# Optimization experiments

Measured on AMD Instinct MI355X. Metric: run time of the kernel, lower is better.

## Reference

```python
import jax, jax.numpy as jnp
import numpy as np

VAR0, VAR1 = 0.1, 0.2          # SSD variances
IOU_THRESH = 0.5
NUM_CLASSES = 21
NEGPOS_RATIO = 3
ALPHA = 1.0


def mid_to_corner(b):
    # [cx,cy,w,h] -> [xmin,ymin,xmax,ymax]
    return jnp.concatenate([b[:, :2] - b[:, 2:] / 2, b[:, :2] + b[:, 2:] / 2], axis=1)


def jaccard(box_a, box_b):
    # box_a [n,4], box_b [P,4] corner form -> IoU [n,P]
    lt = jnp.maximum(box_a[:, None, :2], box_b[None, :, :2])
    rb = jnp.minimum(box_a[:, None, 2:], box_b[None, :, 2:])
    wh = jnp.clip(rb - lt, 0.0)
    inter = wh[..., 0] * wh[..., 1]
    area_a = (box_a[:, 2] - box_a[:, 0]) * (box_a[:, 3] - box_a[:, 1])
    area_b = (box_b[:, 2] - box_b[:, 0]) * (box_b[:, 3] - box_b[:, 1])
    union = area_a[:, None] + area_b[None, :] - inter
    return inter / union


def encode_offset(matched, priors):
    # matched corner form [P,4], priors center form [P,4]
    g_cxcy = ((matched[:, :2] + matched[:, 2:]) / 2 - priors[:, :2]) / (VAR0 * priors[:, 2:])
    g_wh = jnp.log((matched[:, 2:] - matched[:, :2]) / priors[:, 2:]) / VAR1
    return jnp.concatenate([g_cxcy, g_wh], axis=1)


def match_one(gt_box, gt_cls, valid, priors_corner, priors_mid):
    # gt_box [n,4], gt_cls [n], valid [n] bool; priors [P,4]
    n = gt_box.shape[0]
    P = priors_corner.shape[0]
    ovl = jaccard(gt_box, priors_corner)                    # [n,P]
    ovl = jnp.where(valid[:, None], ovl, -1.0)              # mask padded GTs
    best_truth_idx = jnp.argmax(ovl, axis=0)                # [P]
    best_truth_ovl = jnp.max(ovl, axis=0)                   # [P]
    best_prior_idx = jnp.argmax(ovl, axis=1)                # [n]
    bpi = jnp.where(valid, best_prior_idx, P)               # OOB for padded -> dropped
    best_truth_ovl = best_truth_ovl.at[bpi].set(2.0, mode='drop')
    best_truth_idx = best_truth_idx.at[bpi].set(jnp.arange(n), mode='drop')
    matches = gt_box[best_truth_idx]                        # [P,4]
    loc = encode_offset(matches, priors_mid)                # [P,4]
    conf = gt_cls[best_truth_idx].astype(jnp.int32) + 1     # [P]
    conf = jnp.where(best_truth_ovl < IOU_THRESH, 0, conf)
    return loc, conf


def setup_inputs() -> dict:
    key = jax.random.key(0)
    k = jax.random.split(key, 8)
    B, P, C, NMAX = 64, 8732, 21, 50
    confidence = jax.random.normal(k[0], (B, P, C), dtype=jnp.float32)
    location = 0.1 * jax.random.normal(k[1], (B, P, 4), dtype=jnp.float32)
    cxcy = jax.random.uniform(k[2], (P, 2), minval=0.05, maxval=0.95)
    pwh = jax.random.uniform(k[3], (P, 2), minval=0.05, maxval=0.4)
    prior_boxes = jnp.concatenate([cxcy, pwh], axis=1).astype(jnp.float32)
    xymin = jax.random.uniform(k[4], (B, NMAX, 2), minval=0.0, maxval=0.6)
    gwh = jax.random.uniform(k[5], (B, NMAX, 2), minval=0.05, maxval=0.35)
    cls = jax.random.randint(k[6], (B, NMAX), 0, C - 1).astype(jnp.float32)
    labels = jnp.concatenate([xymin, xymin + gwh, cls[..., None]], axis=-1).astype(jnp.float32)
    obj_count = jax.random.randint(k[7], (B, 1), 1, NMAX + 1).astype(jnp.int32)
    return {"confidence": confidence, "location": location,
            "prior_boxes": prior_boxes, "labels": labels, "obj_count": obj_count}


def reference(confidence, location, prior_boxes, labels, obj_count):
    B, P, C = confidence.shape
    NMAX = labels.shape[1]
    priors_corner = mid_to_corner(prior_boxes)
    valid = jnp.arange(NMAX)[None, :] < obj_count            # [B,NMAX]
    loc_t, conf_t = jax.vmap(match_one, in_axes=(0, 0, 0, None, None))(
        labels[..., :4], labels[..., 4], valid, priors_corner, prior_boxes)
    # loc_t [B,P,4] float, conf_t [B,P] int32

    pos = conf_t > 0                                          # [B,P]
    # smooth-L1 over positive anchors (sum reduction)
    d = jnp.abs(location - loc_t)
    sl1 = jnp.where(d < 1.0, 0.5 * d * d, d - 0.5)
    loss_loc = jnp.sum(sl1 * pos[..., None].astype(sl1.dtype))

    # hard negative mining score: global-max logsumexp minus target logit
    bc = confidence.reshape(-1, C)
    x_max = jnp.max(bc)
    lse = jnp.log(jnp.sum(jnp.exp(bc - x_max), axis=1)) + x_max
    tgt_logit = jnp.take_along_axis(bc, conf_t.reshape(-1, 1), axis=1)[:, 0]
    loss_c = (lse - tgt_logit).reshape(B, P)
    loss_c = jnp.where(pos, 0.0, loss_c)
    loss_idx = jnp.argsort(-loss_c, axis=1)                   # descending sort
    idx_rank = jnp.argsort(loss_idx, axis=1)
    num_pos = jnp.sum(pos.astype(jnp.int32), axis=1, keepdims=True)   # [B,1]
    num_neg = jnp.clip(NEGPOS_RATIO * num_pos, None, P - 1)
    neg = idx_rank < num_neg                                  # [B,P]

    # standard cross entropy over selected (pos|neg) anchors, sum reduction
    logp = jax.nn.log_softmax(confidence, axis=-1)            # [B,P,C]
    nll = -jnp.take_along_axis(logp, conf_t[..., None], axis=-1)[..., 0]
    sel = jnp.logical_or(pos, neg)
    loss_conf = jnp.sum(nll * sel.astype(nll.dtype))

    N = jnp.sum(num_pos).astype(confidence.dtype)
    return (ALPHA * loss_loc / N, loss_conf / N)
```

## Files before the change

### kernel.cpp

```cpp
#include <hip/hip_runtime.h>
#include <math.h>

#define Bn 64
#define Pn 8732
#define Cn 21
#define NMAXn 50
#define PX 35

template <int C>
__device__ __forceinline__ float dppf(float x) {
    return __int_as_float(__builtin_amdgcn_update_dpp(0, __float_as_int(x), C, 0xf, 0xf, true));
}
template <int C>
__device__ __forceinline__ int dppi(int x) {
    return __builtin_amdgcn_update_dpp(0, x, C, 0xf, 0xf, true);
}
__device__ __forceinline__ float wave_max_f(float x) {
    x = fmaxf(x, dppf<0x111>(x)); x = fmaxf(x, dppf<0x112>(x));
    x = fmaxf(x, dppf<0x114>(x)); x = fmaxf(x, dppf<0x118>(x));
    x = fmaxf(x, dppf<0x142>(x)); x = fmaxf(x, dppf<0x143>(x));
    return x;
}
__device__ __forceinline__ float wave_sum_f(float x) {
    x += dppf<0x111>(x); x += dppf<0x112>(x); x += dppf<0x114>(x);
    x += dppf<0x118>(x); x += dppf<0x142>(x); x += dppf<0x143>(x);
    return x;
}
__device__ __forceinline__ int wave_sum_i(int x) {
    x += dppi<0x111>(x); x += dppi<0x112>(x); x += dppi<0x114>(x);
    x += dppi<0x118>(x); x += dppi<0x142>(x); x += dppi<0x143>(x);
    return x;
}

__global__ __launch_bounds__(256) void k_bpp(const float* __restrict__ labels,
                                             const int* __restrict__ objc,
                                             const float* __restrict__ priors,
                                             int* __restrict__ match,
                                             unsigned long long* __restrict__ bpk) {
    const int b = blockIdx.y;
    const int px = blockIdx.x;
    const int tid = threadIdx.x;
    const int lane = tid & 63, wid = tid >> 6;
    const int cnt = objc[b];
    const float* lb = labels + b * NMAXn * 5;

    const int p = px * 256 + tid;
    const bool valid = p < Pn;
    const int pcl = valid ? p : (Pn - 1);
    const float4 pr = reinterpret_cast<const float4*>(priors)[pcl];
    const float px0 = pr.x - 0.5f * pr.z, py0 = pr.y - 0.5f * pr.w;
    const float px1 = pr.x + 0.5f * pr.z, py1 = pr.y + 0.5f * pr.w;
    const float parea = (px1 - px0) * (py1 - py0);

    float best = -1.0f;
    int bidx = 0;
    for (int n = 0; n < cnt; ++n) {
        const float gx0 = lb[n * 5 + 0], gy0 = lb[n * 5 + 1];
        const float gx1 = lb[n * 5 + 2], gy1 = lb[n * 5 + 3];
        const float lx = fmaxf(gx0, px0), ly = fmaxf(gy0, py0);
        const float rx = fminf(gx1, px1), ry = fminf(gy1, py1);
        const float w = fmaxf(rx - lx, 0.0f), h = fmaxf(ry - ly, 0.0f);
        const float inter = w * h;
        const float ga = (gx1 - gx0) * (gy1 - gy0);
        const float q = inter / (ga + parea - inter);
        if (q > best) { best = q; bidx = n; }
        const float qr = valid ? q : 0.0f;
        const float m = wave_max_f(qr);
        const float s_q = __int_as_float(__builtin_amdgcn_readlane(__float_as_int(m), 63));
        const unsigned long long mask = __ballot(qr == s_q);
        if (lane == 0) {
            const int first = __ffsll(mask) - 1;
            const int pw = px * 256 + (wid << 6) + first;
            const unsigned long long key =
                ((unsigned long long)__float_as_uint(s_q) << 32) |
                (unsigned long long)(65535 - pw);
            bpk[(size_t)(b * NMAXn + n) * (PX * 4) + px * 4 + wid] = key;
        }
    }
    if (valid) match[(size_t)b * Pn + p] = (bidx << 1) | (best >= 0.5f ? 1 : 0);
}

__global__ __launch_bounds__(64) void k_bpr(const int* __restrict__ objc,
                                            const unsigned long long* __restrict__ bpk,
                                            int* __restrict__ match,
                                            int* __restrict__ done) {
    __shared__ int sbp[NMAXn];
    const int b = blockIdx.x;
    const int tid = threadIdx.x;
    if (b == 0 && tid == 0) *done = 0;
    const int cnt = objc[b];
    if (tid < cnt) {
        const size_t g0 = (size_t)(b * NMAXn + tid) * (PX * 4);
        unsigned long long best = 0ull;
        for (int t = 0; t < PX * 4; ++t) {
            const unsigned long long k = bpk[g0 + t];
            best = (k > best) ? k : best;
        }
        sbp[tid] = 65535 - (int)(best & 0xFFFFull);
    }
    __syncthreads();
    if (tid < cnt) {
        const int myp = sbp[tid];
        bool win = true;
        for (int n2 = tid + 1; n2 < cnt; ++n2) win = win && (sbp[n2] != myp);
        if (win) match[(size_t)b * Pn + myp] = (tid << 1) | 1;
    }
}

__global__ __launch_bounds__(256) void k_main(const float* __restrict__ conf,
                                              const float* __restrict__ loc,
                                              const float* __restrict__ priors,
                                              const float* __restrict__ labels,
                                              const int* __restrict__ match,
                                              float* __restrict__ lc,
                                              float* __restrict__ part_loc,
                                              float* __restrict__ part_nll,
                                              int* __restrict__ part_np) {
    const int b = blockIdx.y;
    const int px = blockIdx.x;
    const int p0 = px * 256;
    const int tid = threadIdx.x;
    const int rows = min(256, Pn - p0);
    const int p = p0 + ((tid < rows) ? tid : 0);
    const size_t gi = (size_t)b * Pn + p;
    const int w = match[gi];

    __shared__ float sconf[256 * Cn];
    __shared__ float lab[NMAXn * 5];
    const float4* src = reinterpret_cast<const float4*>(conf + ((size_t)b * Pn + p0) * Cn);
    const int n4 = rows * Cn / 4;
    for (int i = tid; i < n4; i += 256) reinterpret_cast<float4*>(sconf)[i] = src[i];
    for (int i = tid; i < NMAXn * 5; i += 256) lab[i] = labels[b * NMAXn * 5 + i];
    __syncthreads();

    float my_loc = 0.0f, my_nll = 0.0f;
    int my_np = 0;
    if (tid < rows) {
        const int ti = w >> 1;
        const int ct = (w & 1) ? ((int)lab[ti * 5 + 4] + 1) : 0;
        const float* row = sconf + tid * Cn;
        float m = row[0];
#pragma unroll
        for (int j = 1; j < Cn; ++j) m = fmaxf(m, row[j]);
        float s2 = 0.0f;
#pragma unroll
        for (int j = 0; j < Cn; ++j) s2 += __expf(row[j] - m);
        const float nll = __logf(s2) + m - row[ct];
        if (ct > 0) {
            lc[gi] = 0.0f;
            my_np = 1;
            my_nll = nll;
            const float4 pr = reinterpret_cast<const float4*>(priors)[p];
            const float gx0 = lab[ti * 5 + 0], gy0 = lab[ti * 5 + 1];
            const float gx1 = lab[ti * 5 + 2], gy1 = lab[ti * 5 + 3];
            const float tx = ((gx0 + gx1) * 0.5f - pr.x) / (0.1f * pr.z);
            const float ty = ((gy0 + gy1) * 0.5f - pr.y) / (0.1f * pr.w);
            const float tw = __logf((gx1 - gx0) / pr.z) * 5.0f;
            const float th = __logf((gy1 - gy0) / pr.w) * 5.0f;
            const float4 l = reinterpret_cast<const float4*>(loc)[gi];
            float d;
            d = fabsf(l.x - tx); my_loc += (d < 1.0f) ? 0.5f * d * d : d - 0.5f;
            d = fabsf(l.y - ty); my_loc += (d < 1.0f) ? 0.5f * d * d : d - 0.5f;
            d = fabsf(l.z - tw); my_loc += (d < 1.0f) ? 0.5f * d * d : d - 0.5f;
            d = fabsf(l.w - th); my_loc += (d < 1.0f) ? 0.5f * d * d : d - 0.5f;
        } else {
            lc[gi] = nll;
        }
    }
    my_loc = wave_sum_f(my_loc);
    my_nll = wave_sum_f(my_nll);
    my_np = wave_sum_i(my_np);
    __shared__ float rl[4], rn[4];
    __shared__ int rp[4];
    const int wid = tid >> 6, lane = tid & 63;
    if (lane == 63) { rl[wid] = my_loc; rn[wid] = my_nll; rp[wid] = my_np; }
    __syncthreads();
    if (tid == 0) {
        const int g = b * PX + px;
        part_loc[g] = rl[0] + rl[1] + rl[2] + rl[3];
        part_nll[g] = rn[0] + rn[1] + rn[2] + rn[3];
        part_np[g] = rp[0] + rp[1] + rp[2] + rp[3];
    }
}

__global__ __launch_bounds__(256) void k_neg(const float* __restrict__ lc,
                                             const float* __restrict__ part_loc,
                                             const float* __restrict__ part_nll,
                                             const int* __restrict__ part_np,
                                             float* __restrict__ negsum,
                                             int* __restrict__ done,
                                             float* __restrict__ out) {
    const int b = blockIdx.x;
    const int tid = threadIdx.x;
    const int lane = tid & 63, wid = tid >> 6;
    __shared__ int redc[2][4];
    __shared__ float redf[4], redf2[4];
    __shared__ int redi[4];
    __shared__ int np_sh, islast;

    const int NV = Pn / 4;
    const float4* src = reinterpret_cast<const float4*>(lc + (size_t)b * Pn);
    const float4 sent = make_float4(-1.0f, -1.0f, -1.0f, -1.0f);
    float4 rr[12];
#pragma unroll
    for (int j = 0; j < 12; ++j) {
        const int i = tid + 256 * j;
        rr[j] = (i < NV) ? src[i] : sent;
    }

    if (tid < 64) {
        int npl = (tid < PX) ? part_np[b * PX + tid] : 0;
        npl = wave_sum_i(npl);
        if (tid == 63) np_sh = npl;
    }
    __syncthreads();
    const int k = min(3 * np_sh, Pn - 1);

    unsigned lo = 0u, hi = 0x7F800000u;
#pragma unroll 1
    for (int it = 0; it < 31; ++it) {
        const unsigned mid = lo + ((hi - lo) >> 1);
        const float fm = __uint_as_float(mid);
        int c = 0;
#pragma unroll
        for (int j = 0; j < 12; ++j)
            c += (rr[j].x >= fm) + (rr[j].y >= fm) + (rr[j].z >= fm) + (rr[j].w >= fm);
        c = wave_sum_i(c);
        if (lane == 63) redc[it & 1][wid] = c;
        __syncthreads();
        const int tot = redc[it & 1][0] + redc[it & 1][1]
                      + redc[it & 1][2] + redc[it & 1][3];
        if (tot >= k) lo = mid;
        else hi = mid;
    }
    const float v = __uint_as_float(lo);

    float sm = 0.0f;
    int c = 0;
#pragma unroll
    for (int j = 0; j < 12; ++j) {
        if (rr[j].x > v) { sm += rr[j].x; ++c; }
        if (rr[j].y > v) { sm += rr[j].y; ++c; }
        if (rr[j].z > v) { sm += rr[j].z; ++c; }
        if (rr[j].w > v) { sm += rr[j].w; ++c; }
    }
    sm = wave_sum_f(sm);
    c = wave_sum_i(c);
    if (lane == 63) { redf[wid] = sm; redi[wid] = c; }
    __syncthreads();
    if (tid == 0) {
        const float st = redf[0] + redf[1] + redf[2] + redf[3];
        const int ct = redi[0] + redi[1] + redi[2] + redi[3];
        negsum[b] = st + (float)(k - ct) * v;
        __threadfence();
        islast = (atomicAdd(done, 1) == Bn - 1) ? 1 : 0;
    }
    __syncthreads();
    if (!islast) return;
    __threadfence();

    float sl = 0.0f, sn = 0.0f;
    int np = 0;
    for (int i = tid; i < Bn * PX; i += 256) {
        sl += part_loc[i];
        sn += part_nll[i];
        np += part_np[i];
    }
    if (tid < Bn) sn += negsum[tid];
    sl = wave_sum_f(sl);
    sn = wave_sum_f(sn);
    np = wave_sum_i(np);
    if (lane == 63) { redf[wid] = sn; redf2[wid] = sl; redi[wid] = np; }
    __syncthreads();
    if (tid == 0) {
        const float fN = (float)(redi[0] + redi[1] + redi[2] + redi[3]);
        out[0] = (redf2[0] + redf2[1] + redf2[2] + redf2[3]) / fN;
        out[1] = (redf[0] + redf[1] + redf[2] + redf[3]) / fN;
    }
}

extern "C" void kernel_launch(void* const* d_in, const int* in_sizes, int n_in,
                              void* d_out, int out_size, void* d_ws, size_t ws_size,
                              hipStream_t stream) {
    const float* conf = (const float*)d_in[0];
    const float* loc = (const float*)d_in[1];
    const float* priors = (const float*)d_in[2];
    const float* labels = (const float*)d_in[3];
    const int* objc = (const int*)d_in[4];
    float* out = (float*)d_out;

    unsigned long long* bpk = (unsigned long long*)d_ws;
    float* part_loc = (float*)(bpk + (size_t)Bn * NMAXn * PX * 4);
    float* part_nll = part_loc + Bn * PX;
    int* part_np = (int*)(part_nll + Bn * PX);
    float* negsum = (float*)(part_np + Bn * PX);
    int* match = (int*)(negsum + Bn);
    float* lc = (float*)(match + (size_t)Bn * Pn);
    int* done = (int*)(lc + (size_t)Bn * Pn);

    dim3 g(PX, Bn);
    k_bpp<<<g, 256, 0, stream>>>(labels, objc, priors, match, bpk);
    k_bpr<<<Bn, 64, 0, stream>>>(objc, bpk, match, done);
    k_main<<<g, 256, 0, stream>>>(conf, loc, priors, labels, match, lc,
                                  part_loc, part_nll, part_np);
    k_neg<<<Bn, 256, 0, stream>>>(lc, part_loc, part_nll, part_np, negsum, done, out);
}
```

Before: 79.76 us.

## Fuse prior matching into main loss kernel and apply forced-match fixups as deltas

Merges the per-prior IoU matching kernel with the main softmax/loss kernel, so the match array is no longer written and read back and one launch is removed. The forced best-prior assignments, which previously rewrote the match array before the loss pass, are now handled by a small fixup kernel. It recomputes each affected prior's original match and emits delta corrections to the NLL, localization loss and positive counts, which the negative-mining kernel folds in. This adds per-batch redundant IoU and softmax work in the fixup and makes correctness depend on the delta logic handling overlaps.

```diff
diff --git a/kernel.cpp b/kernel.cpp
--- a/kernel.cpp
+++ b/kernel.cpp
@@ -32,26 +32,56 @@
     return x;
 }
 
-__global__ __launch_bounds__(256) void k_bpp(const float* __restrict__ labels,
-                                             const int* __restrict__ objc,
-                                             const float* __restrict__ priors,
-                                             int* __restrict__ match,
-                                             unsigned long long* __restrict__ bpk) {
+__device__ __forceinline__ float smoothl1_enc(const float4 l, const float4 pr,
+                                              float gx0, float gy0, float gx1, float gy1) {
+    const float tx = ((gx0 + gx1) * 0.5f - pr.x) / (0.1f * pr.z);
+    const float ty = ((gy0 + gy1) * 0.5f - pr.y) / (0.1f * pr.w);
+    const float tw = __logf((gx1 - gx0) / pr.z) * 5.0f;
+    const float th = __logf((gy1 - gy0) / pr.w) * 5.0f;
+    float s = 0.0f, d;
+    d = fabsf(l.x - tx); s += (d < 1.0f) ? 0.5f * d * d : d - 0.5f;
+    d = fabsf(l.y - ty); s += (d < 1.0f) ? 0.5f * d * d : d - 0.5f;
+    d = fabsf(l.z - tw); s += (d < 1.0f) ? 0.5f * d * d : d - 0.5f;
+    d = fabsf(l.w - th); s += (d < 1.0f) ? 0.5f * d * d : d - 0.5f;
+    return s;
+}
+
+__global__ __launch_bounds__(256) void k_fused(const float* __restrict__ conf,
+                                               const float* __restrict__ loc,
+                                               const float* __restrict__ priors,
+                                               const float* __restrict__ labels,
+                                               const int* __restrict__ objc,
+                                               float* __restrict__ lc,
+                                               float* __restrict__ part_loc,
+                                               float* __restrict__ part_nll,
+                                               int* __restrict__ part_np,
+                                               unsigned long long* __restrict__ bpk) {
     const int b = blockIdx.y;
     const int px = blockIdx.x;
+    const int p0 = px * 256;
     const int tid = threadIdx.x;
     const int lane = tid & 63, wid = tid >> 6;
+    const int rows = min(256, Pn - p0);
     const int cnt = objc[b];
     const float* lb = labels + b * NMAXn * 5;
 
-    const int p = px * 256 + tid;
+    __shared__ float sconf[256 * Cn];
+    __shared__ float lab[NMAXn * 5];
+    __shared__ float rl[4], rn[4];
+    __shared__ int rp[4];
+
+    const float4* src = reinterpret_cast<const float4*>(conf + ((size_t)b * Pn + p0) * Cn);
+    const int n4 = rows * Cn / 4;
+    for (int i = tid; i < n4; i += 256) reinterpret_cast<float4*>(sconf)[i] = src[i];
+    for (int i = tid; i < NMAXn * 5; i += 256) lab[i] = labels[b * NMAXn * 5 + i];
+
+    const int p = p0 + tid;
     const bool valid = p < Pn;
     const int pcl = valid ? p : (Pn - 1);
     const float4 pr = reinterpret_cast<const float4*>(priors)[pcl];
     const float px0 = pr.x - 0.5f * pr.z, py0 = pr.y - 0.5f * pr.w;
     const float px1 = pr.x + 0.5f * pr.z, py1 = pr.y + 0.5f * pr.w;
     const float parea = (px1 - px0) * (py1 - py0);
-
     float best = -1.0f;
     int bidx = 0;
     for (int n = 0; n < cnt; ++n) {
@@ -70,74 +100,20 @@
         const unsigned long long mask = __ballot(qr == s_q);
         if (lane == 0) {
             const int first = __ffsll(mask) - 1;
-            const int pw = px * 256 + (wid << 6) + first;
+            const int pw = p0 + (wid << 6) + first;
             const unsigned long long key =
                 ((unsigned long long)__float_as_uint(s_q) << 32) |
                 (unsigned long long)(65535 - pw);
             bpk[(size_t)(b * NMAXn + n) * (PX * 4) + px * 4 + wid] = key;
         }
     }
-    if (valid) match[(size_t)b * Pn + p] = (bidx << 1) | (best >= 0.5f ? 1 : 0);
-}
-
-__global__ __launch_bounds__(64) void k_bpr(const int* __restrict__ objc,
-                                            const unsigned long long* __restrict__ bpk,
-                                            int* __restrict__ match,
-                                            int* __restrict__ done) {
-    __shared__ int sbp[NMAXn];
-    const int b = blockIdx.x;
-    const int tid = threadIdx.x;
-    if (b == 0 && tid == 0) *done = 0;
-    const int cnt = objc[b];
-    if (tid < cnt) {
-        const size_t g0 = (size_t)(b * NMAXn + tid) * (PX * 4);
-        unsigned long long best = 0ull;
-        for (int t = 0; t < PX * 4; ++t) {
-            const unsigned long long k = bpk[g0 + t];
-            best = (k > best) ? k : best;
-        }
-        sbp[tid] = 65535 - (int)(best & 0xFFFFull);
-    }
-    __syncthreads();
-    if (tid < cnt) {
-        const int myp = sbp[tid];
-        bool win = true;
-        for (int n2 = tid + 1; n2 < cnt; ++n2) win = win && (sbp[n2] != myp);
-        if (win) match[(size_t)b * Pn + myp] = (tid << 1) | 1;
-    }
-}
-
-__global__ __launch_bounds__(256) void k_main(const float* __restrict__ conf,
-                                              const float* __restrict__ loc,
-                                              const float* __restrict__ priors,
-                                              const float* __restrict__ labels,
-                                              const int* __restrict__ match,
-                                              float* __restrict__ lc,
-                                              float* __restrict__ part_loc,
-                                              float* __restrict__ part_nll,
-                                              int* __restrict__ part_np) {
-    const int b = blockIdx.y;
-    const int px = blockIdx.x;
-    const int p0 = px * 256;
-    const int tid = threadIdx.x;
-    const int rows = min(256, Pn - p0);
-    const int p = p0 + ((tid < rows) ? tid : 0);
-    const size_t gi = (size_t)b * Pn + p;
-    const int w = match[gi];
-
-    __shared__ float sconf[256 * Cn];
-    __shared__ float lab[NMAXn * 5];
-    const float4* src = reinterpret_cast<const float4*>(conf + ((size_t)b * Pn + p0) * Cn);
-    const int n4 = rows * Cn / 4;
-    for (int i = tid; i < n4; i += 256) reinterpret_cast<float4*>(sconf)[i] = src[i];
-    for (int i = tid; i < NMAXn * 5; i += 256) lab[i] = labels[b * NMAXn * 5 + i];
     __syncthreads();
 
     float my_loc = 0.0f, my_nll = 0.0f;
     int my_np = 0;
     if (tid < rows) {
-        const int ti = w >> 1;
-        const int ct = (w & 1) ? ((int)lab[ti * 5 + 4] + 1) : 0;
+        const size_t gi = (size_t)b * Pn + p;
+        const int ct = (best >= 0.5f) ? ((int)lab[bidx * 5 + 4] + 1) : 0;
         const float* row = sconf + tid * Cn;
         float m = row[0];
 #pragma unroll
@@ -150,19 +126,9 @@
             lc[gi] = 0.0f;
             my_np = 1;
             my_nll = nll;
-            const float4 pr = reinterpret_cast<const float4*>(priors)[p];
-            const float gx0 = lab[ti * 5 + 0], gy0 = lab[ti * 5 + 1];
-            const float gx1 = lab[ti * 5 + 2], gy1 = lab[ti * 5 + 3];
-            const float tx = ((gx0 + gx1) * 0.5f - pr.x) / (0.1f * pr.z);
-            const float ty = ((gy0 + gy1) * 0.5f - pr.y) / (0.1f * pr.w);
-            const float tw = __logf((gx1 - gx0) / pr.z) * 5.0f;
-            const float th = __logf((gy1 - gy0) / pr.w) * 5.0f;
             const float4 l = reinterpret_cast<const float4*>(loc)[gi];
-            float d;
-            d = fabsf(l.x - tx); my_loc += (d < 1.0f) ? 0.5f * d * d : d - 0.5f;
-            d = fabsf(l.y - ty); my_loc += (d < 1.0f) ? 0.5f * d * d : d - 0.5f;
-            d = fabsf(l.z - tw); my_loc += (d < 1.0f) ? 0.5f * d * d : d - 0.5f;
-            d = fabsf(l.w - th); my_loc += (d < 1.0f) ? 0.5f * d * d : d - 0.5f;
+            my_loc = smoothl1_enc(l, pr, lab[bidx * 5 + 0], lab[bidx * 5 + 1],
+                                  lab[bidx * 5 + 2], lab[bidx * 5 + 3]);
         } else {
             lc[gi] = nll;
         }
@@ -170,9 +136,6 @@
     my_loc = wave_sum_f(my_loc);
     my_nll = wave_sum_f(my_nll);
     my_np = wave_sum_i(my_np);
-    __shared__ float rl[4], rn[4];
-    __shared__ int rp[4];
-    const int wid = tid >> 6, lane = tid & 63;
     if (lane == 63) { rl[wid] = my_loc; rn[wid] = my_nll; rp[wid] = my_np; }
     __syncthreads();
     if (tid == 0) {
@@ -183,10 +146,101 @@
     }
 }
 
+__global__ __launch_bounds__(64) void k_fix(const float* __restrict__ conf,
+                                            const float* __restrict__ loc,
+                                            const float* __restrict__ priors,
+                                            const float* __restrict__ labels,
+                                            const int* __restrict__ objc,
+                                            const unsigned long long* __restrict__ bpk,
+                                            float* __restrict__ lc,
+                                            int* __restrict__ fix_np,
+                                            float* __restrict__ fix_nll,
+                                            float* __restrict__ fix_loc,
+                                            int* __restrict__ done) {
+    __shared__ int sbp[NMAXn];
+    __shared__ float lab[NMAXn * 5];
+    const int b = blockIdx.x;
+    const int tid = threadIdx.x;
+    if (b == 0 && tid == 0) *done = 0;
+    const int cnt = objc[b];
+    for (int i = tid; i < NMAXn * 5; i += 64) lab[i] = labels[b * NMAXn * 5 + i];
+    if (tid < cnt) {
+        const size_t g0 = (size_t)(b * NMAXn + tid) * (PX * 4);
+        unsigned long long bestk = 0ull;
+        for (int t = 0; t < PX * 4; ++t) {
+            const unsigned long long k = bpk[g0 + t];
+            bestk = (k > bestk) ? k : bestk;
+        }
+        sbp[tid] = 65535 - (int)(bestk & 0xFFFFull);
+    }
+    __syncthreads();
+    bool win = false;
+    if (tid < cnt) {
+        const int myp = sbp[tid];
+        win = true;
+        for (int n2 = tid + 1; n2 < cnt; ++n2) win = win && (sbp[n2] != myp);
+    }
+    float dnll = 0.0f, dloc = 0.0f;
+    int dnp = 0;
+    if (win) {
+        const int pp = sbp[tid];
+        const float4 prf = reinterpret_cast<const float4*>(priors)[pp];
+        const float qx0 = prf.x - 0.5f * prf.z, qy0 = prf.y - 0.5f * prf.w;
+        const float qx1 = prf.x + 0.5f * prf.z, qy1 = prf.y + 0.5f * prf.w;
+        const float qarea = (qx1 - qx0) * (qy1 - qy0);
+        float best2 = -1.0f;
+        int bidx2 = 0;
+        for (int n2 = 0; n2 < cnt; ++n2) {
+            const float gx0 = lab[n2 * 5 + 0], gy0 = lab[n2 * 5 + 1];
+            const float gx1 = lab[n2 * 5 + 2], gy1 = lab[n2 * 5 + 3];
+            const float lx = fmaxf(gx0, qx0), ly = fmaxf(gy0, qy0);
+            const float rx = fminf(gx1, qx1), ry = fminf(gy1, qy1);
+            const float w = fmaxf(rx - lx, 0.0f), h = fmaxf(ry - ly, 0.0f);
+            const float inter = w * h;
+            const float ga = (gx1 - gx0) * (gy1 - gy0);
+            const float q = inter / (ga + qarea - inter);
+            if (q > best2) { best2 = q; bidx2 = n2; }
+        }
+        const float* rowg = conf + ((size_t)b * Pn + pp) * Cn;
+        float m2 = rowg[0];
+#pragma unroll
+        for (int j = 1; j < Cn; ++j) m2 = fmaxf(m2, rowg[j]);
+        float ss = 0.0f;
+#pragma unroll
+        for (int j = 0; j < Cn; ++j) ss += __expf(rowg[j] - m2);
+        const float lse = __logf(ss) + m2;
+        const int ctn = (int)lab[tid * 5 + 4] + 1;
+        const float4 lv = reinterpret_cast<const float4*>(loc)[(size_t)b * Pn + pp];
+        dnll = lse - rowg[ctn];
+        dloc = smoothl1_enc(lv, prf, lab[tid * 5 + 0], lab[tid * 5 + 1],
+                            lab[tid * 5 + 2], lab[tid * 5 + 3]);
+        dnp = 1;
+        if (best2 >= 0.5f) {
+            const int cto = (int)lab[bidx2 * 5 + 4] + 1;
+            dnll -= (lse - rowg[cto]);
+            dloc -= smoothl1_enc(lv, prf, lab[bidx2 * 5 + 0], lab[bidx2 * 5 + 1],
+                                 lab[bidx2 * 5 + 2], lab[bidx2 * 5 + 3]);
+            dnp = 0;
+        }
+        lc[(size_t)b * Pn + pp] = 0.0f;
+    }
+    dnll = wave_sum_f(dnll);
+    dloc = wave_sum_f(dloc);
+    dnp = wave_sum_i(dnp);
+    if (tid == 63) {
+        fix_nll[b] = dnll;
+        fix_loc[b] = dloc;
+        fix_np[b] = dnp;
+    }
+}
+
 __global__ __launch_bounds__(256) void k_neg(const float* __restrict__ lc,
                                              const float* __restrict__ part_loc,
                                              const float* __restrict__ part_nll,
                                              const int* __restrict__ part_np,
+                                             const int* __restrict__ fix_np,
+                                             const float* __restrict__ fix_nll,
+                                             const float* __restrict__ fix_loc,
                                              float* __restrict__ negsum,
                                              int* __restrict__ done,
                                              float* __restrict__ out) {
@@ -214,7 +268,7 @@
         if (tid == 63) np_sh = npl;
     }
     __syncthreads();
-    const int k = min(3 * np_sh, Pn - 1);
+    const int k = min(3 * (np_sh + fix_np[b]), Pn - 1);
 
     unsigned lo = 0u, hi = 0x7F800000u;
 #pragma unroll 1
@@ -266,7 +320,11 @@
         sn += part_nll[i];
         np += part_np[i];
     }
-    if (tid < Bn) sn += negsum[tid];
+    if (tid < Bn) {
+        sn += negsum[tid] + fix_nll[tid];
+        sl += fix_loc[tid];
+        np += fix_np[tid];
+    }
     sl = wave_sum_f(sl);
     sn = wave_sum_f(sn);
     np = wave_sum_i(np);
@@ -294,14 +352,17 @@
     float* part_nll = part_loc + Bn * PX;
     int* part_np = (int*)(part_nll + Bn * PX);
     float* negsum = (float*)(part_np + Bn * PX);
-    int* match = (int*)(negsum + Bn);
-    float* lc = (float*)(match + (size_t)Bn * Pn);
+    int* fix_np = (int*)(negsum + Bn);
+    float* fix_nll = (float*)(fix_np + Bn);
+    float* fix_loc = fix_nll + Bn;
+    float* lc = fix_loc + Bn;
     int* done = (int*)(lc + (size_t)Bn * Pn);
 
     dim3 g(PX, Bn);
-    k_bpp<<<g, 256, 0, stream>>>(labels, objc, priors, match, bpk);
-    k_bpr<<<Bn, 64, 0, stream>>>(objc, bpk, match, done);
-    k_main<<<g, 256, 0, stream>>>(conf, loc, priors, labels, match, lc,
-                                  part_loc, part_nll, part_np);
-    k_neg<<<Bn, 256, 0, stream>>>(lc, part_loc, part_nll, part_np, negsum, done, out);
-}
+    k_fused<<<g, 256, 0, stream>>>(conf, loc, priors, labels, objc, lc,
+                                   part_loc, part_nll, part_np, bpk);
+    k_fix<<<Bn, 64, 0, stream>>>(conf, loc, priors, labels, objc, bpk, lc,
+                                 fix_np, fix_nll, fix_loc, done);
+    k_neg<<<Bn, 256, 0, stream>>>(lc, part_loc, part_nll, part_np,
+                                  fix_np, fix_nll, fix_loc, negsum, done, out);
+}
```

New measurement: 84.71 us. 6.2% more time.
